# Kernel tuning notes

Hardware: AMD Instinct MI355X
Metric: run time of the kernel (lower is better)

## Reference

```python
import jax, jax.numpy as jnp
import numpy as np

COMMITMENT_COST = 0.25


def setup_inputs() -> dict:
    key = jax.random.key(0)
    k1, k2 = jax.random.split(key)
    x = jax.random.normal(k1, (32, 256, 32, 32), dtype=jnp.float32)
    codebook = jax.random.normal(k2, (1024, 256), dtype=jnp.float32) * 0.02
    return {"x": x, "codebook": codebook}


def reference(x, codebook):
    # x: [B, C, H, W] -> z: [B, H, W, C] (NHWC), C = embedding_dim
    B, C, H, W = x.shape
    z = jnp.transpose(x, (0, 2, 3, 1))
    zf = z.reshape(-1, C)  # [N, C], N = B*H*W
    # squared euclidean distance: ||z||^2 - 2 z.e + ||e||^2  -> [N, K]
    d = (
        jnp.sum(zf * zf, axis=-1, keepdims=True)
        - 2.0 * (zf @ codebook.T)
        + jnp.sum(codebook * codebook, axis=-1)
    )
    encoding_indices = jnp.argmin(d, axis=1)  # [N]
    quantized = codebook[encoding_indices].reshape(z.shape)  # [B, H, W, C]

    # training losses (entropy_loss_ratio == 0 -> entropy branch skipped)
    sg = jax.lax.stop_gradient
    e_latent_loss = jnp.mean((sg(quantized) - z) ** 2) * COMMITMENT_COST
    q_latent_loss = jnp.mean((quantized - sg(z)) ** 2)
    quantizer_loss = e_latent_loss + q_latent_loss

    # straight-through estimator
    quantized_st = z + sg(quantized - z)
    out = jnp.transpose(quantized_st, (0, 3, 1, 2))  # back to NCHW
    return out, quantizer_loss, e_latent_loss, q_latent_loss, encoding_indices
```

## Files before the change

kernel.cpp:

```cpp
#include <hip/hip_runtime.h>
#include <cfloat>

#define C_DIM   256
#define HW      1024
#define N_ROWS  32768
#define K_CODES 1024
#define ROWS    64
#define NCHUNK  32
#define CHUNK_BYTES 16384
#define LISTCAP 128
#define DELTA   0.008f
#define CMASK   0xFFFFFFE0u
#define ZSTRIDE 260

#define OUT_ELEMS 8388608
#define LOSS_OFF  8388608
#define IDX_OFF   8388611

typedef _Float16 half8 __attribute__((ext_vector_type(8)));
typedef _Float16 f16x4 __attribute__((ext_vector_type(4)));
typedef float    f32x4 __attribute__((ext_vector_type(4)));

#define AS1 __attribute__((address_space(1)))
#define AS3 __attribute__((address_space(3)))

#define OFF_EBUF  0
#define OFF_EN    66560
#define OFF_S32   70656
#define OFF_M1W   70912
#define OFF_THR   71424
#define OFF_RES   71680
#define OFF_FIDX  72192
#define OFF_LCNT  72448
#define OFF_LMETA 72704
#define SMEM_BYTES 74752

#define QT_STRIDE 258

#define DPP_MIN(x, ctrl) fminf((x), __int_as_float(__builtin_amdgcn_update_dpp(0, __float_as_int(x), (ctrl), 0xf, 0xf, true)))

__global__ void prep_kernel(const float* __restrict__ cb, float* __restrict__ enorm,
                            char* __restrict__ cb16) {
    int k = blockIdx.x * 4 + (threadIdx.x >> 6);
    int lane = threadIdx.x & 63;
    int c0 = lane * 4;
    float4 v = *(const float4*)(cb + k * C_DIM + c0);
    double s = (double)v.x * v.x + (double)v.y * v.y + (double)v.z * v.z + (double)v.w * v.w;
    #pragma unroll
    for (int m = 1; m < 64; m <<= 1) s += __shfl_xor(s, m, 64);
    if (lane == 0) enorm[k] = (float)s;
    f16x4 h;
    h[0] = (_Float16)v.x; h[1] = (_Float16)v.y; h[2] = (_Float16)v.z; h[3] = (_Float16)v.w;
    int dst = ((k >> 4) << 13) + ((c0 >> 5) << 10) + (((c0 >> 3) & 3) << 8)
            + ((k & 15) << 4) + ((c0 & 7) << 1);
    *(f16x4*)(cb16 + dst) = h;
}

__global__ __launch_bounds__(256, 2) void vq_main(
    const float* __restrict__ x, const float* __restrict__ cb,
    const float* __restrict__ enorm_g, const char* __restrict__ cb16,
    float* __restrict__ out, float* __restrict__ idx_out, float* __restrict__ t2_out)
{
    extern __shared__ char smem[];
    float* zt      = (float*)(smem + OFF_EBUF);
    float* qt      = (float*)(smem + OFF_EBUF);
    char*  ebuf    = smem + OFF_EBUF;
    float* en_lds  = (float*)(smem + OFF_EN);
    float* S32     = (float*)(smem + OFF_S32);
    float* m1w     = (float*)(smem + OFF_M1W);
    float* thr     = (float*)(smem + OFF_THR);
    unsigned long long* res = (unsigned long long*)(smem + OFF_RES);
    int*   fidx    = (int*)(smem + OFF_FIDX);
    int*   lcnt    = (int*)(smem + OFF_LCNT);
    unsigned int* lmeta = (unsigned int*)(smem + OFF_LMETA);

    const int t    = threadIdx.x;
    const int lane = t & 63;
    const int wv   = t >> 6;
    const int wr   = wv >> 1;
    const int wc   = wv & 1;
    const int l15  = lane & 15;
    const int l4   = lane >> 4;
    const int row0 = blockIdx.x * ROWS;
    const int b    = row0 >> 10;
    const int hw0  = row0 & 1023;
    const float* xb = x + b * (C_DIM * HW) + hw0;

    const int qofs = (wc << 13) + (wr << 12);

    {
        int g   = t & 15;
        int cb4 = t >> 4;
        for (int cc = cb4 * 4; cc < C_DIM; cc += 64) {
            float4 v0 = *(const float4*)(xb + (cc + 0) * HW + g * 4);
            float4 v1 = *(const float4*)(xb + (cc + 1) * HW + g * 4);
            float4 v2 = *(const float4*)(xb + (cc + 2) * HW + g * 4);
            float4 v3 = *(const float4*)(xb + (cc + 3) * HW + g * 4);
            *(float4*)&zt[(g * 4 + 0) * ZSTRIDE + cc] = make_float4(v0.x, v1.x, v2.x, v3.x);
            *(float4*)&zt[(g * 4 + 1) * ZSTRIDE + cc] = make_float4(v0.y, v1.y, v2.y, v3.y);
            *(float4*)&zt[(g * 4 + 2) * ZSTRIDE + cc] = make_float4(v0.z, v1.z, v2.z, v3.z);
            *(float4*)&zt[(g * 4 + 3) * ZSTRIDE + cc] = make_float4(v0.w, v1.w, v2.w, v3.w);
        }
        *(float4*)&en_lds[t * 4] = *(const float4*)(enorm_g + t * 4);
        if (t < 4) lcnt[t] = 0;
    }
    __syncthreads();

    {
        int r = t >> 2, seg = t & 3;
        const float* zr = &zt[r * ZSTRIDE + seg * 64];
        double s = 0.0;
        for (int c = 0; c < 64; c += 4) {
            float4 v = *(const float4*)(zr + c);
            s = fma((double)v.x, (double)v.x, s);
            s = fma((double)v.y, (double)v.y, s);
            s = fma((double)v.z, (double)v.z, s);
            s = fma((double)v.w, (double)v.w, s);
        }
        s += __shfl_xor(s, 1, 64);
        s += __shfl_xor(s, 2, 64);
        if (seg == 0) S32[r] = (float)s;
    }

    half8 af[2][8];
    #pragma unroll
    for (int rt = 0; rt < 2; rt++) {
        int row = wr * 32 + rt * 16 + l15;
        #pragma unroll
        for (int kk = 0; kk < 8; kk++) {
            int c0 = kk * 32 + l4 * 8;
            float4 a  = *(const float4*)&zt[row * ZSTRIDE + c0];
            float4 a2 = *(const float4*)&zt[row * ZSTRIDE + c0 + 4];
            half8 h;
            h[0] = (_Float16)(-2.0f * a.x);  h[1] = (_Float16)(-2.0f * a.y);
            h[2] = (_Float16)(-2.0f * a.z);  h[3] = (_Float16)(-2.0f * a.w);
            h[4] = (_Float16)(-2.0f * a2.x); h[5] = (_Float16)(-2.0f * a2.y);
            h[6] = (_Float16)(-2.0f * a2.z); h[7] = (_Float16)(-2.0f * a2.w);
            af[rt][kk] = h;
        }
    }
    __syncthreads();

    #pragma unroll
    for (int c2 = 0; c2 < 2; c2++) {
        const char* src = cb16 + c2 * CHUNK_BYTES + qofs;
        char* dst = ebuf + c2 * CHUNK_BYTES + qofs;
        #pragma unroll
        for (int i = 0; i < 4; i++) {
            __builtin_amdgcn_global_load_lds((const AS1 unsigned int*)(src + i * 1024 + lane * 16),
                                             (AS3 unsigned int*)(dst + i * 1024), 16, 0, 0);
        }
    }

    const int bbase  = (wc << 13) + (l4 << 8) + (l15 << 4);
    const int enbase = wc * 16 + l15;

    float u1[2][4], u2[2][4];
    #pragma unroll
    for (int rt = 0; rt < 2; rt++)
        #pragma unroll
        for (int r2 = 0; r2 < 4; r2++) { u1[rt][r2] = FLT_MAX; u2[rt][r2] = FLT_MAX; }

    int r3 = 0;
    for (int ch = 0; ch < NCHUNK; ch++) {
        if (ch == NCHUNK - 1) { asm volatile("s_waitcnt vmcnt(0)" ::: "memory"); }
        else                  { asm volatile("s_waitcnt vmcnt(4)" ::: "memory"); }
        __builtin_amdgcn_sched_barrier(0);
        __builtin_amdgcn_s_barrier();
        __builtin_amdgcn_sched_barrier(0);

        const char* ebc = ebuf + r3 * CHUNK_BYTES;
        half8 bf[8];
        #pragma unroll
        for (int kk = 0; kk < 8; kk++)
            bf[kk] = *(const half8*)(ebc + bbase + (kk << 10));

        if (ch + 2 < NCHUNK) {
            int w3 = r3 + 2; if (w3 >= 3) w3 -= 3;
            const char* src = cb16 + (ch + 2) * CHUNK_BYTES + qofs;
            char* dst = ebuf + w3 * CHUNK_BYTES + qofs;
            #pragma unroll
            for (int i = 0; i < 4; i++) {
                __builtin_amdgcn_global_load_lds((const AS1 unsigned int*)(src + i * 1024 + lane * 16),
                                                 (AS3 unsigned int*)(dst + i * 1024), 16, 0, 0);
            }
        }

        const float en = en_lds[enbase + ch * 32];
        f32x4 acc0 = {en, en, en, en};
        f32x4 acc1 = {en, en, en, en};
        #pragma unroll
        for (int kk = 0; kk < 8; kk++) {
            acc0 = __builtin_amdgcn_mfma_f32_16x16x32_f16(af[0][kk], bf[kk], acc0, 0, 0, 0);
            acc1 = __builtin_amdgcn_mfma_f32_16x16x32_f16(af[1][kk], bf[kk], acc1, 0, 0, 0);
        }
        #pragma unroll
        for (int r2 = 0; r2 < 4; r2++) {
            float a0 = __uint_as_float((__float_as_uint(acc0[r2]) & CMASK) | (unsigned)ch);
            u2[0][r2] = __builtin_amdgcn_fmed3f(a0, u1[0][r2], u2[0][r2]);
            u1[0][r2] = fminf(u1[0][r2], a0);
            float a1 = __uint_as_float((__float_as_uint(acc1[r2]) & CMASK) | (unsigned)ch);
            u2[1][r2] = __builtin_amdgcn_fmed3f(a1, u1[1][r2], u2[1][r2]);
            u1[1][r2] = fminf(u1[1][r2], a1);
        }

        r3 += 1; if (r3 >= 3) r3 -= 3;
    }

    #pragma unroll
    for (int rt = 0; rt < 2; rt++) {
        #pragma unroll
        for (int r2 = 0; r2 < 4; r2++) {
            float m = u1[rt][r2];
            m = DPP_MIN(m, 0xB1);
            m = DPP_MIN(m, 0x4E);
            m = DPP_MIN(m, 0x141);
            m = DPP_MIN(m, 0x140);
            if (l15 == 0) m1w[wc * 64 + wr * 32 + rt * 16 + l4 * 4 + r2] = m;
        }
    }
    __syncthreads();
    if (t < 64) {
        thr[t] = fminf(m1w[t], m1w[64 + t]) + DELTA;
        res[t] = ~0ull;
    }
    __syncthreads();

    #pragma unroll
    for (int rt = 0; rt < 2; rt++) {
        #pragma unroll
        for (int r2 = 0; r2 < 4; r2++) {
            int row_l = wr * 32 + rt * 16 + l4 * 4 + r2;
            float tr = thr[row_l];
            if (u1[rt][r2] < tr) {
                int ch1 = (int)(__float_as_uint(u1[rt][r2]) & 31u);
                int code = ch1 * 32 + wc * 16 + l15;
                int slot = atomicAdd(&lcnt[wv], 1);
                if (slot < LISTCAP)
                    lmeta[wv * LISTCAP + slot] = ((unsigned)row_l << 16) | (unsigned)code;
            }
            if (u2[rt][r2] < tr) {
                int ch2 = (int)(__float_as_uint(u2[rt][r2]) & 31u);
                int code = ch2 * 32 + wc * 16 + l15;
                int slot = atomicAdd(&lcnt[wv], 1);
                if (slot < LISTCAP)
                    lmeta[wv * LISTCAP + slot] = ((unsigned)row_l << 16) | (unsigned)code;
            }
        }
    }
    __syncthreads();

    {
        int n = lcnt[wv]; if (n > LISTCAP) n = LISTCAP;
        for (int base = 0; base < n; base += 4) {
            int it = base + l4;
            if (it < n) {
                unsigned meta = lmeta[wv * LISTCAP + it];
                int row  = (int)(meta >> 16);
                int code = (int)(meta & 1023u);
                const float* xr = xb + row;
                const float* er = cb + code * C_DIM;
                double acc = 0.0;
                #pragma unroll
                for (int s2 = 0; s2 < 16; s2++) {
                    int c = l15 + 16 * s2;
                    acc = fma((double)xr[(size_t)c * HW], (double)er[c], acc);
                }
                acc += __shfl_xor(acc, 1, 64);
                acc += __shfl_xor(acc, 2, 64);
                acc += __shfl_xor(acc, 4, 64);
                acc += __shfl_xor(acc, 8, 64);
                if (l15 == 0) {
                    float Mf = (float)acc;
                    float t2 = __fadd_rn(__fsub_rn(S32[row], __fmul_rn(2.0f, Mf)), en_lds[code]);
                    unsigned long long pk =
                        ((unsigned long long)__float_as_uint(t2) << 32) | (unsigned long long)(unsigned)code;
                    atomicMin(&res[row], pk);
                }
            }
        }
    }
    __syncthreads();

    if (t < 64) {
        unsigned long long v = res[t];
        int code = (int)(v & 1023u);
        fidx[t] = code;
        idx_out[row0 + t] = (float)code;
        t2_out[row0 + t] = __uint_as_float((unsigned)(v >> 32));
    }

    float* ob = out + b * (C_DIM * HW) + hw0;
    #pragma unroll
    for (int half = 0; half < 2; half++) {
        __syncthreads();
        for (int idx = t; idx < 32 * 64; idx += 256) {
            int r  = idx >> 6;
            int c4 = idx & 63;
            const float* er = cb + fidx[half * 32 + r] * C_DIM;
            *(float4*)&qt[r * QT_STRIDE + c4 * 4] = *(const float4*)(er + c4 * 4);
        }
        __syncthreads();
        int rr = t & 31;
        int cg = t >> 5;
        for (int cc = cg; cc < C_DIM; cc += 8) {
            ob[cc * HW + half * 32 + rr] = qt[rr * QT_STRIDE + cc];
        }
    }
}

__global__ void loss_kernel(const float* __restrict__ t2min, float* __restrict__ losses) {
    __shared__ double sh[256];
    int t = threadIdx.x;
    double a = 0.0;
    const int per = N_ROWS / 256;
    for (int i = t * per; i < t * per + per; i++) a += (double)t2min[i];
    sh[t] = a;
    __syncthreads();
    for (int s = 128; s > 0; s >>= 1) {
        if (t < s) sh[t] += sh[t + s];
        __syncthreads();
    }
    if (t == 0) {
        double M = sh[0] / (double)OUT_ELEMS;
        losses[0] = (float)(1.25 * M);
        losses[1] = (float)(0.25 * M);
        losses[2] = (float)(M);
    }
}

extern "C" void kernel_launch(void* const* d_in, const int* in_sizes, int n_in,
                              void* d_out, int out_size, void* d_ws, size_t ws_size,
                              hipStream_t stream) {
    const float* x  = (const float*)d_in[0];
    const float* cb = (const float*)d_in[1];
    float* out     = (float*)d_out;
    float* losses  = out + LOSS_OFF;
    float* idx_out = out + IDX_OFF;

    char*  cb16     = (char*)d_ws;
    float* t2ws     = (float*)((char*)d_ws + 524288);
    float* enorm_ws = (float*)((char*)d_ws + 524288 + 131072);

    hipFuncSetAttribute(reinterpret_cast<const void*>(vq_main),
                        hipFuncAttributeMaxDynamicSharedMemorySize, SMEM_BYTES);

    prep_kernel<<<K_CODES / 4, 256, 0, stream>>>(cb, enorm_ws, cb16);
    vq_main<<<N_ROWS / ROWS, 256, SMEM_BYTES, stream>>>(x, cb, enorm_ws, cb16, out, idx_out, t2ws);
    loss_kernel<<<1, 256, 0, stream>>>(t2ws, losses);
}
```

Before: 65.91 us.

## Split 64-row block across 8 waves with one 16-row MFMA tile each

Doubles the block to 512 threads so each of 8 waves handles a 16-row tile instead of two, halving per-wave accumulators, A fragments and async codebook loads. The cooperative loads, wait counts, list counters and output loops are adjusted to match. The goal is more waves in flight to hide LDS and memory latency and to cut register pressure. The cost is more waves reading the same B fragments from LDS and heavier barrier synchronisation, and LDS use grows slightly, which may limit how many blocks fit per CU.

```diff
diff --git a/kernel.cpp b/kernel.cpp
--- a/kernel.cpp
+++ b/kernel.cpp
@@ -33,7 +33,7 @@
 #define OFF_FIDX  72192
 #define OFF_LCNT  72448
 #define OFF_LMETA 72704
-#define SMEM_BYTES 74752
+#define SMEM_BYTES 76800
 
 #define QT_STRIDE 258
 
@@ -56,7 +56,7 @@
     *(f16x4*)(cb16 + dst) = h;
 }
 
-__global__ __launch_bounds__(256, 2) void vq_main(
+__global__ __launch_bounds__(512, 4) void vq_main(
     const float* __restrict__ x, const float* __restrict__ cb,
     const float* __restrict__ enorm_g, const char* __restrict__ cb16,
     float* __restrict__ out, float* __restrict__ idx_out, float* __restrict__ t2_out)
@@ -86,12 +86,12 @@
     const int hw0  = row0 & 1023;
     const float* xb = x + b * (C_DIM * HW) + hw0;
 
-    const int qofs = (wc << 13) + (wr << 12);
+    const int qofs = wv * 2048;
 
     {
         int g   = t & 15;
         int cb4 = t >> 4;
-        for (int cc = cb4 * 4; cc < C_DIM; cc += 64) {
+        for (int cc = cb4 * 4; cc < C_DIM; cc += 128) {
             float4 v0 = *(const float4*)(xb + (cc + 0) * HW + g * 4);
             float4 v1 = *(const float4*)(xb + (cc + 1) * HW + g * 4);
             float4 v2 = *(const float4*)(xb + (cc + 2) * HW + g * 4);
@@ -101,12 +101,12 @@
             *(float4*)&zt[(g * 4 + 2) * ZSTRIDE + cc] = make_float4(v0.z, v1.z, v2.z, v3.z);
             *(float4*)&zt[(g * 4 + 3) * ZSTRIDE + cc] = make_float4(v0.w, v1.w, v2.w, v3.w);
         }
-        *(float4*)&en_lds[t * 4] = *(const float4*)(enorm_g + t * 4);
-        if (t < 4) lcnt[t] = 0;
-    }
-    __syncthreads();
-
-    {
+        if (t < 256) *(float4*)&en_lds[t * 4] = *(const float4*)(enorm_g + t * 4);
+        if (t < 8) lcnt[t] = 0;
+    }
+    __syncthreads();
+
+    if (t < 256) {
         int r = t >> 2, seg = t & 3;
         const float* zr = &zt[r * ZSTRIDE + seg * 64];
         double s = 0.0;
@@ -122,10 +122,9 @@
         if (seg == 0) S32[r] = (float)s;
     }
 
-    half8 af[2][8];
-    #pragma unroll
-    for (int rt = 0; rt < 2; rt++) {
-        int row = wr * 32 + rt * 16 + l15;
+    half8 af[8];
+    {
+        int row = wr * 16 + l15;
         #pragma unroll
         for (int kk = 0; kk < 8; kk++) {
             int c0 = kk * 32 + l4 * 8;
@@ -136,7 +135,7 @@
             h[2] = (_Float16)(-2.0f * a.z);  h[3] = (_Float16)(-2.0f * a.w);
             h[4] = (_Float16)(-2.0f * a2.x); h[5] = (_Float16)(-2.0f * a2.y);
             h[6] = (_Float16)(-2.0f * a2.z); h[7] = (_Float16)(-2.0f * a2.w);
-            af[rt][kk] = h;
+            af[kk] = h;
         }
     }
     __syncthreads();
@@ -146,7 +145,7 @@
         const char* src = cb16 + c2 * CHUNK_BYTES + qofs;
         char* dst = ebuf + c2 * CHUNK_BYTES + qofs;
         #pragma unroll
-        for (int i = 0; i < 4; i++) {
+        for (int i = 0; i < 2; i++) {
             __builtin_amdgcn_global_load_lds((const AS1 unsigned int*)(src + i * 1024 + lane * 16),
                                              (AS3 unsigned int*)(dst + i * 1024), 16, 0, 0);
         }
@@ -155,16 +154,14 @@
     const int bbase  = (wc << 13) + (l4 << 8) + (l15 << 4);
     const int enbase = wc * 16 + l15;
 
-    float u1[2][4], u2[2][4];
-    #pragma unroll
-    for (int rt = 0; rt < 2; rt++)
-        #pragma unroll
-        for (int r2 = 0; r2 < 4; r2++) { u1[rt][r2] = FLT_MAX; u2[rt][r2] = FLT_MAX; }
+    float u1[4], u2[4];
+    #pragma unroll
+    for (int r2 = 0; r2 < 4; r2++) { u1[r2] = FLT_MAX; u2[r2] = FLT_MAX; }
 
     int r3 = 0;
     for (int ch = 0; ch < NCHUNK; ch++) {
         if (ch == NCHUNK - 1) { asm volatile("s_waitcnt vmcnt(0)" ::: "memory"); }
-        else                  { asm volatile("s_waitcnt vmcnt(4)" ::: "memory"); }
+        else                  { asm volatile("s_waitcnt vmcnt(2)" ::: "memory"); }
         __builtin_amdgcn_sched_barrier(0);
         __builtin_amdgcn_s_barrier();
         __builtin_amdgcn_sched_barrier(0);
@@ -180,44 +177,36 @@
             const char* src = cb16 + (ch + 2) * CHUNK_BYTES + qofs;
             char* dst = ebuf + w3 * CHUNK_BYTES + qofs;
             #pragma unroll
-            for (int i = 0; i < 4; i++) {
+            for (int i = 0; i < 2; i++) {
                 __builtin_amdgcn_global_load_lds((const AS1 unsigned int*)(src + i * 1024 + lane * 16),
                                                  (AS3 unsigned int*)(dst + i * 1024), 16, 0, 0);
             }
         }
 
         const float en = en_lds[enbase + ch * 32];
-        f32x4 acc0 = {en, en, en, en};
-        f32x4 acc1 = {en, en, en, en};
-        #pragma unroll
-        for (int kk = 0; kk < 8; kk++) {
-            acc0 = __builtin_amdgcn_mfma_f32_16x16x32_f16(af[0][kk], bf[kk], acc0, 0, 0, 0);
-            acc1 = __builtin_amdgcn_mfma_f32_16x16x32_f16(af[1][kk], bf[kk], acc1, 0, 0, 0);
-        }
+        f32x4 acc = {en, en, en, en};
+        #pragma unroll
+        for (int kk = 0; kk < 8; kk++)
+            acc = __builtin_amdgcn_mfma_f32_16x16x32_f16(af[kk], bf[kk], acc, 0, 0, 0);
+
         #pragma unroll
         for (int r2 = 0; r2 < 4; r2++) {
-            float a0 = __uint_as_float((__float_as_uint(acc0[r2]) & CMASK) | (unsigned)ch);
-            u2[0][r2] = __builtin_amdgcn_fmed3f(a0, u1[0][r2], u2[0][r2]);
-            u1[0][r2] = fminf(u1[0][r2], a0);
-            float a1 = __uint_as_float((__float_as_uint(acc1[r2]) & CMASK) | (unsigned)ch);
-            u2[1][r2] = __builtin_amdgcn_fmed3f(a1, u1[1][r2], u2[1][r2]);
-            u1[1][r2] = fminf(u1[1][r2], a1);
+            float a0 = __uint_as_float((__float_as_uint(acc[r2]) & CMASK) | (unsigned)ch);
+            u2[r2] = __builtin_amdgcn_fmed3f(a0, u1[r2], u2[r2]);
+            u1[r2] = fminf(u1[r2], a0);
         }
 
         r3 += 1; if (r3 >= 3) r3 -= 3;
     }
 
     #pragma unroll
-    for (int rt = 0; rt < 2; rt++) {
-        #pragma unroll
-        for (int r2 = 0; r2 < 4; r2++) {
-            float m = u1[rt][r2];
-            m = DPP_MIN(m, 0xB1);
-            m = DPP_MIN(m, 0x4E);
-            m = DPP_MIN(m, 0x141);
-            m = DPP_MIN(m, 0x140);
-            if (l15 == 0) m1w[wc * 64 + wr * 32 + rt * 16 + l4 * 4 + r2] = m;
-        }
+    for (int r2 = 0; r2 < 4; r2++) {
+        float m = u1[r2];
+        m = DPP_MIN(m, 0xB1);
+        m = DPP_MIN(m, 0x4E);
+        m = DPP_MIN(m, 0x141);
+        m = DPP_MIN(m, 0x140);
+        if (l15 == 0) m1w[wc * 64 + wr * 16 + l4 * 4 + r2] = m;
     }
     __syncthreads();
     if (t < 64) {
@@ -227,25 +216,22 @@
     __syncthreads();
 
     #pragma unroll
-    for (int rt = 0; rt < 2; rt++) {
-        #pragma unroll
-        for (int r2 = 0; r2 < 4; r2++) {
-            int row_l = wr * 32 + rt * 16 + l4 * 4 + r2;
-            float tr = thr[row_l];
-            if (u1[rt][r2] < tr) {
-                int ch1 = (int)(__float_as_uint(u1[rt][r2]) & 31u);
-                int code = ch1 * 32 + wc * 16 + l15;
-                int slot = atomicAdd(&lcnt[wv], 1);
-                if (slot < LISTCAP)
-                    lmeta[wv * LISTCAP + slot] = ((unsigned)row_l << 16) | (unsigned)code;
-            }
-            if (u2[rt][r2] < tr) {
-                int ch2 = (int)(__float_as_uint(u2[rt][r2]) & 31u);
-                int code = ch2 * 32 + wc * 16 + l15;
-                int slot = atomicAdd(&lcnt[wv], 1);
-                if (slot < LISTCAP)
-                    lmeta[wv * LISTCAP + slot] = ((unsigned)row_l << 16) | (unsigned)code;
-            }
+    for (int r2 = 0; r2 < 4; r2++) {
+        int row_l = wr * 16 + l4 * 4 + r2;
+        float tr = thr[row_l];
+        if (u1[r2] < tr) {
+            int ch1 = (int)(__float_as_uint(u1[r2]) & 31u);
+            int code = ch1 * 32 + wc * 16 + l15;
+            int slot = atomicAdd(&lcnt[wv], 1);
+            if (slot < LISTCAP)
+                lmeta[wv * LISTCAP + slot] = ((unsigned)row_l << 16) | (unsigned)code;
+        }
+        if (u2[r2] < tr) {
+            int ch2 = (int)(__float_as_uint(u2[r2]) & 31u);
+            int code = ch2 * 32 + wc * 16 + l15;
+            int slot = atomicAdd(&lcnt[wv], 1);
+            if (slot < LISTCAP)
+                lmeta[wv * LISTCAP + slot] = ((unsigned)row_l << 16) | (unsigned)code;
         }
     }
     __syncthreads();
@@ -294,7 +280,7 @@
     #pragma unroll
     for (int half = 0; half < 2; half++) {
         __syncthreads();
-        for (int idx = t; idx < 32 * 64; idx += 256) {
+        for (int idx = t; idx < 32 * 64; idx += 512) {
             int r  = idx >> 6;
             int c4 = idx & 63;
             const float* er = cb + fidx[half * 32 + r] * C_DIM;
@@ -303,7 +289,7 @@
         __syncthreads();
         int rr = t & 31;
         int cg = t >> 5;
-        for (int cc = cg; cc < C_DIM; cc += 8) {
+        for (int cc = cg; cc < C_DIM; cc += 16) {
             ob[cc * HW + half * 32 + rr] = qt[rr * QT_STRIDE + cc];
         }
     }
@@ -346,6 +332,6 @@
                         hipFuncAttributeMaxDynamicSharedMemorySize, SMEM_BYTES);
 
     prep_kernel<<<K_CODES / 4, 256, 0, stream>>>(cb, enorm_ws, cb16);
-    vq_main<<<N_ROWS / ROWS, 256, SMEM_BYTES, stream>>>(x, cb, enorm_ws, cb16, out, idx_out, t2ws);
+    vq_main<<<N_ROWS / ROWS, 512, SMEM_BYTES, stream>>>(x, cb, enorm_ws, cb16, out, idx_out, t2ws);
     loss_kernel<<<1, 256, 0, stream>>>(t2ws, losses);
 }
```

New measurement: 65.32 us. Within noise of the previous version (-0.9%).
